# Performance work log

Measured on AMD Instinct MI355X. Metric: run time of the kernel, lower is better.

## Reference

```python
import jax, jax.numpy as jnp
import numpy as np

B, K, N, T, C = 2, 2, 4096, 8, 3
H = 192            # hidden_dim
NODE_DIM = 10
N_LAYERS = 10
KNN = 16           # k nearest neighbours
TOP_FRAC = 0.4
SHARP = 5.0        # mask_sharpness
S = max(int(TOP_FRAC * N), KNN + 1)   # n_select per graph


def _ln(x, g, b, eps=1e-5):
    mu = x.mean(-1, keepdims=True)
    v = ((x - mu) ** 2).mean(-1, keepdims=True)  # biased var, matches nn.LayerNorm
    return (x - mu) / jnp.sqrt(v + eps) * g + b


def setup_inputs() -> dict:
    key = jax.random.key(0)
    ks = jax.random.split(key, 12)
    rn = lambda k, shape: 0.05 * jax.random.normal(k, shape, jnp.float32)
    F0 = 2 * NODE_DIM + 4   # first EdgeConv MLP in-dim
    FR = 2 * H + 4          # remaining EdgeConv MLP in-dim
    L = N_LAYERS - 1
    return {
        "u_base": jax.random.normal(ks[0], (B, K, N, C), jnp.float32),
        "pos": jax.random.uniform(ks[1], (B, N, 3), dtype=jnp.float32),
        "velocity_in": jax.random.normal(ks[2], (B, T, N, C), jnp.float32),
        "airfoil_mask": (jax.random.uniform(ks[3], (B, N)) < 0.05).astype(jnp.float32),
        "conv0_w1": rn(ks[4], (F0, H)), "conv0_b1": jnp.zeros((H,)),
        "conv0_w2": rn(ks[5], (H, H)), "conv0_b2": jnp.zeros((H,)),
        "conv0_g": jnp.ones((H,)), "conv0_be": jnp.zeros((H,)),
        "convs_w1": rn(ks[6], (L, FR, H)), "convs_b1": jnp.zeros((L, H)),
        "convs_w2": rn(ks[7], (L, H, H)), "convs_b2": jnp.zeros((L, H)),
        "convs_g": jnp.ones((L, H)), "convs_be": jnp.zeros((L, H)),
        "head_g": jnp.ones((H,)), "head_be": jnp.zeros((H,)),
        "head_w1": rn(ks[8], (H, H)), "head_b1": jnp.zeros((H,)),
        "head_w2": rn(ks[9], (H, 3)), "head_b2": jnp.zeros((3,)),
    }


def reference(u_base, pos, velocity_in, airfoil_mask,
              conv0_w1, conv0_b1, conv0_w2, conv0_b2, conv0_g, conv0_be,
              convs_w1, convs_b1, convs_w2, convs_b2, convs_g, convs_be,
              head_g, head_be, head_w1, head_b1, head_w2, head_b2):
    # --- variance gating (torch .var/.std are unbiased) ---
    var_pp = jnp.var(velocity_in, axis=1, ddof=1).sum(-1)                      # [B,N]
    var_z = (var_pp - var_pp.mean(1, keepdims=True)) / (
        jnp.std(var_pp, axis=1, ddof=1, keepdims=True) + 1e-8)
    soft_mask = jax.nn.sigmoid(SHARP * var_z) * (1.0 - airfoil_mask)           # [B,N]

    # --- select top-variance points per graph ---
    _, top_idx = jax.lax.top_k(var_pp, S)                                      # [B,S]
    pos_sel = jnp.take_along_axis(pos, top_idx[..., None], axis=1)             # [B,S,3]
    mask_sel = jnp.take_along_axis(soft_mask, top_idx, axis=1)[..., None]      # [B,S,1]
    v_last = velocity_in[:, -1]                                                # [B,N,C]
    ub_sel = jnp.take_along_axis(u_base, top_idx[:, None, :, None], axis=2)    # [B,K,S,C]
    vl_sel = jnp.take_along_axis(v_last, top_idx[..., None], axis=1)           # [B,S,C]
    vf_sel = jnp.take_along_axis(var_pp[..., None], top_idx[..., None], axis=1)
    static = jnp.concatenate([vl_sel, pos_sel, vf_sel], -1)                    # [B,S,7]
    x0 = jnp.concatenate(
        [ub_sel, jnp.broadcast_to(static[:, None], (B, K, S, 7))], -1)         # [B,K,S,10]

    def per_graph(x, pos_b):  # x: [K,S,F0], pos_b: [S,3]
        # kNN graph (self excluded via +inf diagonal, as in the chunked cdist)
        d2 = jnp.sum((pos_b[:, None] - pos_b[None]) ** 2, -1)                  # [S,S]
        d2 = d2.at[jnp.arange(S), jnp.arange(S)].set(jnp.inf)
        _, knn = jax.lax.top_k(-d2, KNN)                                       # [S,KNN]
        # PyG convention with edge_index=stack([targets, sources]):
        # i = edge_index[1] = knn neighbours, j = edge_index[0] = centre nodes
        idx_i = knn.reshape(-1)                     # [E] aggregation targets
        idx_j = jnp.repeat(jnp.arange(S), KNN)      # [E]
        rel = pos_b[idx_i] - pos_b[idx_j]           # pos[edge_index[1]] - pos[edge_index[0]]
        dist = jnp.linalg.norm(rel, axis=-1, keepdims=True)
        ea = jnp.concatenate([rel, dist], -1)       # [E,4]
        ea_b = jnp.broadcast_to(ea, (K,) + ea.shape)

        def conv(h, w1, b1, w2, b2, g, be):
            hi = h[:, idx_i]
            hj = h[:, idx_j]
            m = jnp.concatenate([hi, hj - hi, ea_b], -1)                       # [K,E,2F+4]
            m = jax.nn.gelu(m @ w1 + b1, approximate=False) @ w2 + b2          # [K,E,H]
            agg = jnp.zeros((K, S, H), h.dtype).at[:, idx_i].add(m)
            return _ln(agg, g, be)

        h = conv(x, conv0_w1, conv0_b1, conv0_w2, conv0_b2, conv0_g, conv0_be)
        for l in range(N_LAYERS - 1):
            h = conv(h, convs_w1[l], convs_b1[l], convs_w2[l], convs_b2[l],
                     convs_g[l], convs_be[l]) + h
        hh = _ln(h, head_g, head_be)
        return jax.nn.gelu(hh @ head_w1 + head_b1, approximate=False) @ head_w2 + head_b2

    delta = jax.vmap(per_graph)(x0, pos_sel)        # [B,K,S,3]
    delta = delta * mask_sel[:, None]               # [B,1,S,1]

    def scatter_b(idx, d):  # idx [S], d [K,S,3]
        return jnp.zeros((K, N, C), d.dtype).at[:, idx].set(d)

    delta_full = jax.vmap(scatter_b)(top_idx, delta)            # [B,K,N,C]
    return (u_base + delta_full) * (1.0 - airfoil_mask)[:, None, :, None]
```

## Files before the change

kernel.cpp:

```cpp
#include <hip/hip_runtime.h>
#include <hip/hip_bf16.h>
#include <math.h>

#define B_ 2
#define K_ 2
#define NN_ 4096
#define T_ 8
#define C_ 3
#define H_ 192
#define S_ 1638
#define KK_ 16
#define E_ (S_*KK_)
#define NROW (B_*K_*S_)
#define SHARP_ 5.0f

typedef __hip_bfloat16 bf;
typedef unsigned long long ull;
typedef __bf16 bf16x8 __attribute__((ext_vector_type(8)));
typedef float f32x4 __attribute__((ext_vector_type(4)));

__device__ int   g_isbf16;
__device__ int   g_viol;
__device__ __align__(16) float g_var[B_*NN_];
__device__ __align__(16) float g_accum[B_*2];
__device__ __align__(16) int   g_topidx[B_*S_];
__device__ __align__(16) float g_possel[B_*S_*3];
__device__ __align__(16) float g_masksel[B_*S_];
__device__ __align__(16) float g_x0[NROW*10];
__device__ __align__(16) int   g_knn[B_*E_];
__device__ __align__(16) float g_ea[B_*E_*4];
__device__ __align__(16) int   g_indeg[B_*S_];
__device__ __align__(16) int   g_cursor[B_*S_];
__device__ __align__(16) int   g_off[B_*(S_+1)];
__device__ __align__(16) int   g_list[B_*E_];
__device__ __align__(16) float g_P[(size_t)NROW*H_];
__device__ __align__(16) bf    g_Qbf[(size_t)NROW*H_];
__device__ __align__(16) float g_h[(size_t)NROW*H_];
__device__ __align__(16) bf    g_hbf[(size_t)NROW*H_];
__device__ __align__(16) bf    g_abf[(size_t)NROW*H_];
__device__ __align__(16) bf    g_hh[(size_t)NROW*H_];
__device__ __align__(16) bf    g_t[(size_t)NROW*H_];
__device__ __align__(16) bf    g_w2p[(size_t)11*H_*H_];
__device__ __align__(16) bf    g_wcp[(size_t)9*H_*384];

__device__ __forceinline__ float bf2f(bf x){ return __bfloat162float(x); }
__device__ __forceinline__ float LD(const void* p, long i){
  return g_isbf16 ? __bfloat162float(((const bf*)p)[i]) : ((const float*)p)[i];
}
__device__ __forceinline__ float gelu_f(float x){ return 0.5f*x*(1.0f + erff(x*0.70710678118654752f)); }
__device__ __forceinline__ ull shfl_xor_u64(ull v, int m){
  unsigned lo = (unsigned)v, hi = (unsigned)(v >> 32);
  lo = __shfl_xor(lo, m, 64); hi = __shfl_xor(hi, m, 64);
  return ((ull)hi << 32) | lo;
}

__global__ void k_vz(const void* a, const void* b, const void* c){
  int tid = blockIdx.x*256 + threadIdx.x;
  if (tid < B_*S_){ g_indeg[tid]=0; g_cursor[tid]=0; }
  if (tid < B_*2) g_accum[tid]=0.f;
  if (blockIdx.x == 0){
    int t = threadIdx.x;
    const bf* pa = (const bf*)a; const bf* pb = (const bf*)b; const bf* pc = (const bf*)c;
    int bad = 0;
    #pragma unroll
    for (int s = 0; s < 2; ++s){
      float va = __bfloat162float(pa[t + s*256]);
      float vb = __bfloat162float(pb[t + s*256]);
      float vc = __bfloat162float(pc[t + s*256]);
      if (!(fabsf(va) <= 1000.f)) bad = 1;
      if (!(fabsf(vb) <= 1000.f)) bad = 1;
      if (!(fabsf(vc) <= 1000.f)) bad = 1;
    }
    if (threadIdx.x == 0) g_viol = 0;
    __syncthreads();
    if (bad) atomicOr(&g_viol, 1);
    __syncthreads();
    if (threadIdx.x == 0) g_isbf16 = (g_viol == 0) ? 1 : 0;
  }
}

__global__ void k_var(const void* __restrict__ vel){
  int b = blockIdx.y;
  int n = blockIdx.x*256 + threadIdx.x;
  float v = 0.f;
  #pragma unroll
  for (int c = 0; c < 3; ++c){
    float x[8];
    #pragma unroll
    for (int t = 0; t < 8; ++t)
      x[t] = LD(vel, ((long)(b*T_+t)*NN_ + n)*3 + c);
    float m = __fadd_rn(__fadd_rn(__fadd_rn(x[0],x[1]), __fadd_rn(x[2],x[3])),
                        __fadd_rn(__fadd_rn(x[4],x[5]), __fadd_rn(x[6],x[7]))) / 8.0f;
    float d[8];
    #pragma unroll
    for (int t = 0; t < 8; ++t){ float dd = __fadd_rn(x[t], -m); d[t] = __fmul_rn(dd,dd); }
    float sv = __fadd_rn(__fadd_rn(__fadd_rn(d[0],d[1]), __fadd_rn(d[2],d[3])),
                         __fadd_rn(__fadd_rn(d[4],d[5]), __fadd_rn(d[6],d[7])));
    v = __fadd_rn(v, sv / 7.0f);
  }
  g_var[b*NN_ + n] = v;
  float s1 = v, s2 = v*v;
  #pragma unroll
  for (int o = 32; o; o >>= 1){ s1 += __shfl_xor(s1,o,64); s2 += __shfl_xor(s2,o,64); }
  __shared__ float r1[4], r2[4];
  int lane = threadIdx.x & 63, wid = threadIdx.x >> 6;
  if (!lane){ r1[wid]=s1; r2[wid]=s2; }
  __syncthreads();
  if (threadIdx.x == 0){
    atomicAdd(&g_accum[b*2+0], r1[0]+r1[1]+r1[2]+r1[3]);
    atomicAdd(&g_accum[b*2+1], r2[0]+r2[1]+r2[2]+r2[3]);
  }
}

__global__ __launch_bounds__(256) void k_rank(){
  int b = blockIdx.y;
  int i = blockIdx.x*4 + (threadIdx.x >> 6);
  int lane = threadIdx.x & 63;
  float vi = g_var[b*NN_+i];
  int rank = 0;
  for (int j = lane; j < NN_; j += 64){
    float vj = g_var[b*NN_+j];
    rank += ((vj > vi) || (vj == vi && j < i)) ? 1 : 0;
  }
  #pragma unroll
  for (int o = 32; o; o >>= 1) rank += __shfl_xor(rank, o, 64);
  if (lane == 0 && rank < S_) g_topidx[b*S_ + rank] = i;
}

__global__ void k_gather(const void* __restrict__ pos, const void* __restrict__ ub,
                         const void* __restrict__ vel, const void* __restrict__ air){
  int gi = blockIdx.x*256 + threadIdx.x;
  if (gi >= B_*S_) return;
  int b = gi / S_, s = gi - b*S_;
  int node = g_topidx[gi];
  float px = LD(pos, ((long)b*NN_+node)*3+0);
  float py = LD(pos, ((long)b*NN_+node)*3+1);
  float pz = LD(pos, ((long)b*NN_+node)*3+2);
  g_possel[gi*3+0]=px; g_possel[gi*3+1]=py; g_possel[gi*3+2]=pz;
  float S1 = g_accum[b*2], S2 = g_accum[b*2+1];
  float mean = S1*(1.f/NN_);
  float sd = sqrtf(fmaxf((S2 - S1*S1*(1.f/NN_))*(1.f/(NN_-1)), 0.f));
  float vf = g_var[b*NN_+node];
  float z = (vf-mean)/(sd+1e-8f);
  float sig = 1.f/(1.f+expf(-SHARP_*z));
  g_masksel[gi] = sig*(1.f - LD(air, b*NN_+node));
  float vl0 = LD(vel, ((long)(b*T_+7)*NN_+node)*3+0);
  float vl1 = LD(vel, ((long)(b*T_+7)*NN_+node)*3+1);
  float vl2 = LD(vel, ((long)(b*T_+7)*NN_+node)*3+2);
  for (int k = 0; k < K_; ++k){
    long row = (long)(b*K_+k)*S_ + s;
    float* x = g_x0 + row*10;
    x[0]=LD(ub, ((long)(b*K_+k)*NN_+node)*3+0);
    x[1]=LD(ub, ((long)(b*K_+k)*NN_+node)*3+1);
    x[2]=LD(ub, ((long)(b*K_+k)*NN_+node)*3+2);
    x[3]=vl0; x[4]=vl1; x[5]=vl2;
    x[6]=px;  x[7]=py;  x[8]=pz;
    x[9]=vf;
  }
}

__global__ __launch_bounds__(256) void k_knn(){
  __shared__ float px[S_], py[S_], pz[S_];
  int b = blockIdx.y;
  int j = blockIdx.x*4 + (threadIdx.x >> 6);
  int lane = threadIdx.x & 63;
  for (int t = threadIdx.x; t < S_; t += 256){
    px[t] = g_possel[(b*S_+t)*3+0];
    py[t] = g_possel[(b*S_+t)*3+1];
    pz[t] = g_possel[(b*S_+t)*3+2];
  }
  __syncthreads();
  if (j >= S_) return;
  float xj=px[j], yj=py[j], zj=pz[j];
  float dist[KK_]; int id[KK_];
  #pragma unroll
  for (int t = 0; t < KK_; ++t){ dist[t]=3.0e38f; id[t]=0x7fffffff; }
  for (int c = lane; c < S_; c += 64){
    if (c == j) continue;
    float dx=__fadd_rn(px[c],-xj), dy=__fadd_rn(py[c],-yj), dz=__fadd_rn(pz[c],-zj);
    float d2 = __fadd_rn(__fadd_rn(__fmul_rn(dx,dx), __fmul_rn(dy,dy)), __fmul_rn(dz,dz));
    if (d2 < dist[KK_-1]){
      int p = 0;
      #pragma unroll
      for (int q = 0; q < KK_; ++q) p += (dist[q] <= d2) ? 1 : 0;
      #pragma unroll
      for (int q = KK_-1; q >= 1; --q){
        bool mv = (q > p);
        dist[q] = mv ? dist[q-1] : dist[q];
        id[q]   = mv ? id[q-1]   : id[q];
      }
      #pragma unroll
      for (int q = 0; q < KK_; ++q){ if (q == p){ dist[q] = d2; id[q] = c; } }
    }
  }
  ull mykey = 0;
  #pragma unroll
  for (int t = 0; t < KK_; ++t){
    ull k = (((ull)__float_as_uint(dist[0])) << 32) | (unsigned)id[0];
    ull m = k;
    #pragma unroll
    for (int o = 32; o; o >>= 1){ ull other = shfl_xor_u64(m, o); m = (other < m) ? other : m; }
    if (k == m){
      #pragma unroll
      for (int q = 0; q < KK_-1; ++q){ dist[q]=dist[q+1]; id[q]=id[q+1]; }
      dist[KK_-1] = 3.0e38f; id[KK_-1] = 0x7fffffff;
    }
    if (lane == t) mykey = m;
  }
  if (lane < KK_){
    int i = (int)(mykey & 0xffffffffu);
    g_knn[(b*S_+j)*KK_ + lane] = i;
    float rx = __fadd_rn(px[i],-xj), ry = __fadd_rn(py[i],-yj), rz = __fadd_rn(pz[i],-zj);
    float dd = sqrtf(__fadd_rn(__fadd_rn(__fmul_rn(rx,rx), __fmul_rn(ry,ry)), __fmul_rn(rz,rz)));
    float* o = g_ea + ((long)b*E_ + j*KK_ + lane)*4;
    o[0]=rx; o[1]=ry; o[2]=rz; o[3]=dd;
    atomicAdd(&g_indeg[b*S_+i], 1);
  }
}

__global__ void k_scan(){
  __shared__ int sA[2048], sB[2048];
  int b = blockIdx.x, tid = threadIdx.x;
  for (int i = tid; i < 2048; i += 1024) sA[i] = (i < S_) ? g_indeg[b*S_+i] : 0;
  __syncthreads();
  int *src = sA, *dst = sB;
  for (int d = 1; d < 2048; d <<= 1){
    for (int i = tid; i < 2048; i += 1024) dst[i] = src[i] + (i >= d ? src[i-d] : 0);
    __syncthreads();
    int* t2 = src; src = dst; dst = t2;
  }
  if (tid == 0) g_off[b*(S_+1)] = 0;
  for (int i = tid; i < S_; i += 1024) g_off[b*(S_+1)+i+1] = src[i];
}

__global__ void k_fill(){
  int idx = blockIdx.x*256 + threadIdx.x;
  if (idx >= B_*E_) return;
  int b = idx / E_, e = idx - b*E_;
  int i = g_knn[idx];
  int slot = atomicAdd(&g_cursor[b*S_+i], 1);
  g_list[b*E_ + g_off[b*(S_+1)+i] + slot] = e;
}

__global__ void k_pack_w2(const void* __restrict__ c0w2, const void* __restrict__ cw2,
                          const void* __restrict__ hw1){
  int gi = blockIdx.x*256 + threadIdx.x;
  if (gi >= 11*H_*H_) return;
  int mat = gi / (H_*H_), r = gi - mat*(H_*H_);
  int k = r / H_, n = r - (r/H_)*H_;
  float v;
  if (mat == 0)      v = LD(c0w2, (long)k*H_ + n);
  else if (mat <= 9) v = LD(cw2, (long)(mat-1)*H_*H_ + (long)k*H_ + n);
  else               v = LD(hw1, (long)k*H_ + n);
  int t = k>>5, q = (k>>3)&3, jj = k&7;
  g_w2p[(size_t)mat*H_*H_ + (((t*4+q)*H_ + n)*8 + jj)] = __float2bfloat16(v);
}

__global__ void k_pack_wc(const void* __restrict__ cw1){
  int gi = blockIdx.x*256 + threadIdx.x;
  if (gi >= 9*H_*384) return;
  int l = gi / (H_*384), r = gi - l*(H_*384);
  int k = r / 384, n = r - (r/384)*384;
  long base = (long)l*388*H_;
  float v;
  if (n < H_) v = LD(cw1, base + (long)k*H_ + n) - LD(cw1, base + (long)(H_+k)*H_ + n);
  else        v = LD(cw1, base + (long)(H_+k)*H_ + (n-H_));
  int t = k>>5, q = (k>>3)&3, jj = k&7;
  g_wcp[(size_t)l*(H_*384) + (((t*4+q)*384 + n)*8 + jj)] = __float2bfloat16(v);
}

__global__ void k_initout(const void* __restrict__ ub, const void* __restrict__ air, float* __restrict__ out){
  int gi = blockIdx.x*256 + threadIdx.x;
  int n = (gi/3) % NN_;
  int b = gi / (K_*NN_*C_);
  float a = 1.f - LD(air, b*NN_+n);
  out[gi] = LD(ub, gi) * a;
}

__global__ __launch_bounds__(256) void k_proj0(const void* __restrict__ w1){
  __shared__ float xs[16][10];
  __shared__ float wP[10][192];
  __shared__ float wQ[10][192];
  int tid = threadIdx.x;
  long rowBase = (long)blockIdx.x * 16;
  for (int idx = tid; idx < 1920; idx += 256){
    int f = idx / 192, n = idx - (idx/192)*192;
    float a = LD(w1, f*H_+n), b = LD(w1, (10+f)*H_+n);
    wP[f][n] = a - b; wQ[f][n] = b;
  }
  for (int idx = tid; idx < 160; idx += 256){
    int r = idx / 10, f = idx - (idx/10)*10;
    long row = rowBase + r; if (row >= NROW) row = NROW-1;
    xs[r][f] = g_x0[row*10 + f];
  }
  __syncthreads();
  for (int o = tid; o < 16*384; o += 256){
    int r = o / 384, n = o - (o/384)*384;
    long row = rowBase + r;
    if (row >= NROW) continue;
    float acc = 0.f;
    if (n < 192){
      #pragma unroll
      for (int f = 0; f < 10; ++f) acc += xs[r][f]*wP[f][n];
      g_P[row*192 + n] = acc;
    } else {
      int nc = n - 192;
      #pragma unroll
      for (int f = 0; f < 10; ++f) acc += xs[r][f]*wQ[f][nc];
      g_Qbf[row*192 + nc] = __float2bfloat16(acc);
    }
  }
}

__global__ __launch_bounds__(256) void k_gemmPQ(int bOff, int M){
  const bf* A  = g_hbf;
  const bf* Bp = g_wcp + bOff;
  int wave = threadIdx.x >> 6, lane = threadIdx.x & 63;
  int q = lane >> 4, l16 = lane & 15;
  long rowBase = (long)blockIdx.x * 16;
  f32x4 acc[6];
  #pragma unroll
  for (int ct = 0; ct < 6; ++ct) acc[ct] = (f32x4){0.f,0.f,0.f,0.f};
  #pragma unroll
  for (int t = 0; t < 6; ++t){
    int kof = t*32 + q*8;
    long r = rowBase + l16; if (r >= M) r = M-1;
    bf16x8 af = *reinterpret_cast<const bf16x8*>(A + r*192 + kof);
    #pragma unroll
    for (int ct = 0; ct < 6; ++ct){
      int n = wave*96 + ct*16 + l16;
      bf16x8 bfr = *reinterpret_cast<const bf16x8*>(Bp + (((t*4+q)*384 + n)*8));
      acc[ct] = __builtin_amdgcn_mfma_f32_16x16x32_bf16(af, bfr, acc[ct], 0,0,0);
    }
  }
  #pragma unroll
  for (int ct = 0; ct < 6; ++ct){
    int col = wave*96 + ct*16 + l16;
    #pragma unroll
    for (int r = 0; r < 4; ++r){
      long row = rowBase + q*4 + r;
      if (row < M){
        float v = acc[ct][r];
        if (col < 192) g_P[row*192 + col] = v;
        else           g_Qbf[row*192 + (col-192)] = __float2bfloat16(v);
      }
    }
  }
}

template<int RES>
__global__ __launch_bounds__(256) void k_gemmln(const void* __restrict__ biasB, long biasO,
                                                const void* __restrict__ gB, long gO,
                                                const void* __restrict__ beB, long beO,
                                                int bOff, int M){
  const bf* A  = g_abf;
  const bf* Bp = g_w2p + bOff;
  int wave = threadIdx.x >> 6, lane = threadIdx.x & 63;
  int q = lane >> 4, l16 = lane & 15;
  long rowBase = (long)blockIdx.x * 16;
  f32x4 acc[3];
  #pragma unroll
  for (int ct = 0; ct < 3; ++ct) acc[ct] = (f32x4){0.f,0.f,0.f,0.f};
  #pragma unroll
  for (int t = 0; t < 6; ++t){
    int kof = t*32 + q*8;
    long r = rowBase + l16; if (r >= M) r = M-1;
    bf16x8 af = *reinterpret_cast<const bf16x8*>(A + r*192 + kof);
    #pragma unroll
    for (int ct = 0; ct < 3; ++ct){
      int n = wave*48 + ct*16 + l16;
      bf16x8 bfr = *reinterpret_cast<const bf16x8*>(Bp + (((t*4+q)*192 + n)*8));
      acc[ct] = __builtin_amdgcn_mfma_f32_16x16x32_bf16(af, bfr, acc[ct], 0,0,0);
    }
  }
  __shared__ float tile[16][200];
  __shared__ float srow[16], rrow[16];
  #pragma unroll
  for (int ct = 0; ct < 3; ++ct){
    int col = wave*48 + ct*16 + l16;
    float bb = LD(biasB, biasO + col);
    #pragma unroll
    for (int r = 0; r < 4; ++r){
      int lr = q*4 + r;
      long row = rowBase + lr;
      long rowc = (row < M) ? row : (M-1);
      int bk = (int)(rowc / S_); int i = (int)(rowc - (long)bk*S_); int b = bk >> 1;
      float degf = (float)(g_off[b*(S_+1)+i+1] - g_off[b*(S_+1)+i]);
      tile[lr][col] = acc[ct][r] + degf*bb;
    }
  }
  __syncthreads();
  {
    int lr = threadIdx.x >> 4;
    int k16 = threadIdx.x & 15;
    float s = 0.f, qq = 0.f;
    for (int c = k16; c < 192; c += 16){ float x = tile[lr][c]; s += x; qq += x*x; }
    #pragma unroll
    for (int o = 1; o < 16; o <<= 1){ s += __shfl_xor(s,o,64); qq += __shfl_xor(qq,o,64); }
    if (k16 == 0){
      float mu = s*(1.f/H_);
      float var = qq*(1.f/H_) - mu*mu;
      srow[lr] = mu;
      rrow[lr] = rsqrtf(fmaxf(var, 0.f) + 1e-5f);
    }
  }
  __syncthreads();
  for (int o = threadIdx.x; o < 16*192; o += 256){
    int lr = o / 192, col = o - (o/192)*192;
    long row = rowBase + lr;
    if (row < M){
      float y = (tile[lr][col] - srow[lr])*rrow[lr]*LD(gB,gO+col) + LD(beB,beO+col);
      if (RES) y += g_h[row*192 + col];
      g_h[row*192 + col] = y;
      g_hbf[row*192 + col] = __float2bfloat16(y);
    }
  }
}

__global__ __launch_bounds__(256) void k_gemmhead(const void* __restrict__ gB,
                                                  const void* __restrict__ beB,
                                                  const void* __restrict__ biasB,
                                                  int bOff, int M){
  const bf* Bp = g_w2p + bOff;
  int wave = threadIdx.x >> 6, lane = threadIdx.x & 63;
  int q = lane >> 4, l16 = lane & 15;
  long rowBase = (long)blockIdx.x * 32;
  __shared__ float tile[32][200];
  __shared__ bf hb_s[32][216];
  __shared__ float srow[32], rrow[32];
  for (int o = threadIdx.x; o < 32*192; o += 256){
    int lr = o / 192, col = o - (o/192)*192;
    long row = rowBase + lr;
    long rowc = (row < M) ? row : (M-1);
    tile[lr][col] = g_h[rowc*192 + col];
  }
  __syncthreads();
  {
    int lr = threadIdx.x >> 3;
    int k8 = threadIdx.x & 7;
    float s = 0.f, qq = 0.f;
    for (int c = k8; c < 192; c += 8){ float x = tile[lr][c]; s += x; qq += x*x; }
    #pragma unroll
    for (int o = 1; o < 8; o <<= 1){ s += __shfl_xor(s,o,64); qq += __shfl_xor(qq,o,64); }
    if (k8 == 0){
      float mu = s*(1.f/H_);
      float var = qq*(1.f/H_) - mu*mu;
      srow[lr] = mu;
      rrow[lr] = rsqrtf(fmaxf(var, 0.f) + 1e-5f);
    }
  }
  __syncthreads();
  for (int o = threadIdx.x; o < 32*192; o += 256){
    int lr = o / 192, col = o - (o/192)*192;
    hb_s[lr][col] = __float2bfloat16((tile[lr][col] - srow[lr])*rrow[lr]*LD(gB,col) + LD(beB,col));
  }
  __syncthreads();
  f32x4 acc[2][3];
  #pragma unroll
  for (int rt = 0; rt < 2; ++rt)
    #pragma unroll
    for (int ct = 0; ct < 3; ++ct) acc[rt][ct] = (f32x4){0.f,0.f,0.f,0.f};
  #pragma unroll
  for (int t = 0; t < 6; ++t){
    int kof = t*32 + q*8;
    bf16x8 af[2], bfr[3];
    #pragma unroll
    for (int rt = 0; rt < 2; ++rt)
      af[rt] = *reinterpret_cast<const bf16x8*>(&hb_s[rt*16 + l16][kof]);
    #pragma unroll
    for (int ct = 0; ct < 3; ++ct){
      int n = wave*48 + ct*16 + l16;
      bfr[ct] = *reinterpret_cast<const bf16x8*>(Bp + (((t*4+q)*192 + n)*8));
    }
    #pragma unroll
    for (int rt = 0; rt < 2; ++rt)
      #pragma unroll
      for (int ct = 0; ct < 3; ++ct)
        acc[rt][ct] = __builtin_amdgcn_mfma_f32_16x16x32_bf16(af[rt], bfr[ct], acc[rt][ct], 0,0,0);
  }
  #pragma unroll
  for (int rt = 0; rt < 2; ++rt){
    #pragma unroll
    for (int ct = 0; ct < 3; ++ct){
      int col = wave*48 + ct*16 + l16;
      float bb = LD(biasB, col);
      #pragma unroll
      for (int r = 0; r < 4; ++r){
        long row = rowBase + rt*16 + q*4 + r;
        if (row < M) g_t[row*192 + col] = __float2bfloat16(gelu_f(acc[rt][ct][r] + bb));
      }
    }
  }
}

__global__ __launch_bounds__(192) void k_aggedge(const void* __restrict__ w1cB, long w1cO,
                                                 const void* __restrict__ b1B, long b1O){
  int row = blockIdx.x;
  int col = threadIdx.x;
  int bk = row / S_, i = row - bk*S_, b = bk >> 1;
  int off = g_off[b*(S_+1)+i];
  int deg = g_off[b*(S_+1)+i+1] - off;
  float w0 = LD(w1cB, w1cO+col),       w1v = LD(w1cB, w1cO+H_+col);
  float w2v = LD(w1cB, w1cO+2*H_+col), w3v = LD(w1cB, w1cO+3*H_+col);
  float base = g_P[(size_t)row*H_ + col] + LD(b1B, b1O+col);
  const int* lst = g_list + b*E_ + off;
  const bf* Q = g_Qbf + (size_t)bk*S_*H_;
  const float* EA = g_ea + (size_t)b*E_*4;
  float acc = 0.f;
  int d = 0;
  for (; d + 4 <= deg; d += 4){
    int e0 = lst[d], e1 = lst[d+1], e2 = lst[d+2], e3 = lst[d+3];
    float4 a0 = *reinterpret_cast<const float4*>(EA + (size_t)e0*4);
    float4 a1 = *reinterpret_cast<const float4*>(EA + (size_t)e1*4);
    float4 a2 = *reinterpret_cast<const float4*>(EA + (size_t)e2*4);
    float4 a3 = *reinterpret_cast<const float4*>(EA + (size_t)e3*4);
    float q0 = bf2f(Q[(size_t)(e0>>4)*H_ + col]);
    float q1 = bf2f(Q[(size_t)(e1>>4)*H_ + col]);
    float q2 = bf2f(Q[(size_t)(e2>>4)*H_ + col]);
    float q3 = bf2f(Q[(size_t)(e3>>4)*H_ + col]);
    acc += gelu_f(base + q0 + a0.x*w0 + a0.y*w1v + a0.z*w2v + a0.w*w3v);
    acc += gelu_f(base + q1 + a1.x*w0 + a1.y*w1v + a1.z*w2v + a1.w*w3v);
    acc += gelu_f(base + q2 + a2.x*w0 + a2.y*w1v + a2.z*w2v + a2.w*w3v);
    acc += gelu_f(base + q3 + a3.x*w0 + a3.y*w1v + a3.z*w2v + a3.w*w3v);
  }
  for (; d < deg; ++d){
    int e = lst[d];
    float4 a = *reinterpret_cast<const float4*>(EA + (size_t)e*4);
    float qv = bf2f(Q[(size_t)(e>>4)*H_ + col]);
    acc += gelu_f(base + qv + a.x*w0 + a.y*w1v + a.z*w2v + a.w*w3v);
  }
  g_abf[(size_t)row*H_ + col] = __float2bfloat16(acc);
}

__global__ void k_headout(const void* __restrict__ w2, const void* __restrict__ b2,
                          const void* __restrict__ ub, const void* __restrict__ air,
                          float* __restrict__ out){
  int row = blockIdx.x*4 + (threadIdx.x >> 6);
  int lane = threadIdx.x & 63;
  if (row >= NROW) return;
  float t0 = bf2f(g_t[(size_t)row*H_ + lane]);
  float t1 = bf2f(g_t[(size_t)row*H_ + lane + 64]);
  float t2 = bf2f(g_t[(size_t)row*H_ + lane + 128]);
  float d[3];
  #pragma unroll
  for (int c = 0; c < 3; ++c){
    float p = t0*LD(w2,lane*3+c) + t1*LD(w2,(lane+64)*3+c) + t2*LD(w2,(lane+128)*3+c);
    #pragma unroll
    for (int o = 32; o; o >>= 1) p += __shfl_xor(p,o,64);
    d[c] = p + LD(b2,c);
  }
  if (lane == 0){
    int bk = row / S_, s = row - bk*S_, b = bk >> 1;
    float msk = g_masksel[b*S_+s];
    int node = g_topidx[b*S_+s];
    float am = 1.f - LD(air, b*NN_+node);
    #pragma unroll
    for (int c = 0; c < 3; ++c){
      long oi = ((long)bk*NN_ + node)*3 + c;
      out[oi] = (LD(ub,oi) + d[c]*msk)*am;
    }
  }
}

extern "C" void kernel_launch(void* const* d_in, const int* in_sizes, int n_in,
                              void* d_out, int out_size, void* d_ws, size_t ws_size,
                              hipStream_t stream) {
  (void)in_sizes; (void)n_in; (void)d_ws; (void)ws_size; (void)out_size;
  const void* u_base = d_in[0];
  const void* pos    = d_in[1];
  const void* vel    = d_in[2];
  const void* air    = d_in[3];
  const void* c0w1   = d_in[4];
  const void* c0b1   = d_in[5];
  const void* c0w2   = d_in[6];
  const void* c0b2   = d_in[7];
  const void* c0g    = d_in[8];
  const void* c0be   = d_in[9];
  const void* cw1    = d_in[10];
  const void* cb1    = d_in[11];
  const void* cw2    = d_in[12];
  const void* cb2    = d_in[13];
  const void* cg     = d_in[14];
  const void* cbe    = d_in[15];
  const void* hg     = d_in[16];
  const void* hbe    = d_in[17];
  const void* hw1    = d_in[18];
  const void* hb1    = d_in[19];
  const void* hw2    = d_in[20];
  const void* hb2    = d_in[21];
  float* out = (float*)d_out;

  k_vz<<<13, 256, 0, stream>>>(u_base, pos, vel);
  k_var<<<dim3(16, B_), 256, 0, stream>>>(vel);
  k_rank<<<dim3(NN_/4, B_), 256, 0, stream>>>();
  k_gather<<<13, 256, 0, stream>>>(pos, u_base, vel, air);
  k_knn<<<dim3((S_+3)/4, B_), 256, 0, stream>>>();
  k_scan<<<B_, 1024, 0, stream>>>();
  k_fill<<<205, 256, 0, stream>>>();
  k_pack_w2<<<1584, 256, 0, stream>>>(c0w2, cw2, hw1);
  k_pack_wc<<<2592, 256, 0, stream>>>(cw1);
  k_initout<<<192, 256, 0, stream>>>(u_base, air, out);
  k_proj0<<<410, 256, 0, stream>>>(c0w1);

  const int GN16 = (NROW + 15) / 16;
  for (int l = 0; l < 10; ++l){
    if (l > 0) k_gemmPQ<<<GN16, 256, 0, stream>>>((l-1)*H_*384, NROW);

    long w1cO = (l == 0) ? 20L*H_ : ((long)(l-1)*388 + 384)*H_;
    const void* w1cB = (l == 0) ? c0w1 : cw1;
    long lOff = (l == 0) ? 0 : (long)(l-1)*H_;
    const void* b1B = (l == 0) ? c0b1 : cb1;
    k_aggedge<<<NROW, 192, 0, stream>>>(w1cB, w1cO, b1B, lOff);

    const void* b2B = (l == 0) ? c0b2 : cb2;
    const void* gB  = (l == 0) ? c0g  : cg;
    const void* beB = (l == 0) ? c0be : cbe;
    if (l > 0) k_gemmln<1><<<GN16, 256, 0, stream>>>(b2B, lOff, gB, lOff, beB, lOff, l*H_*H_, NROW);
    else       k_gemmln<0><<<GN16, 256, 0, stream>>>(b2B, lOff, gB, lOff, beB, lOff, l*H_*H_, NROW);
  }

  k_gemmhead<<<(NROW + 31)/32, 256, 0, stream>>>(hg, hbe, hb1, 10*H_*H_, NROW);
  k_headout<<<NROW/4, 256, 0, stream>>>(hw2, hb2, u_base, air, out);
}
```

Baseline: 659.6 us.

## Fuse next-layer PQ GEMM into LayerNorm kernel and fold head output into head GEMM

The next layer's P/Q projection GEMM now runs inside the LayerNorm kernel, reading the freshly normalized rows from shared memory as bf16 instead of writing g_hbf and launching a separate k_gemmPQ. The final 192->3 head projection and output scatter are fused into the head GEMM kernel, which drops the g_t buffer and the k_headout launch. The dtype check and zeroing move into k_var, which writes per-block partial sums instead of using atomics. The weight pack and output init kernels are merged into one launch. Together this cuts launch count and global round trips, at the cost of more shared memory and registers in the fused kernels.

```diff
diff --git a/kernel.cpp b/kernel.cpp
--- a/kernel.cpp
+++ b/kernel.cpp
@@ -20,9 +20,9 @@
 typedef float f32x4 __attribute__((ext_vector_type(4)));
 
 __device__ int   g_isbf16;
-__device__ int   g_viol;
 __device__ __align__(16) float g_var[B_*NN_];
-__device__ __align__(16) float g_accum[B_*2];
+__device__ __align__(16) float g_vs1[B_*16];
+__device__ __align__(16) float g_vs2[B_*16];
 __device__ __align__(16) int   g_topidx[B_*S_];
 __device__ __align__(16) float g_possel[B_*S_*3];
 __device__ __align__(16) float g_masksel[B_*S_];
@@ -36,16 +36,16 @@
 __device__ __align__(16) float g_P[(size_t)NROW*H_];
 __device__ __align__(16) bf    g_Qbf[(size_t)NROW*H_];
 __device__ __align__(16) float g_h[(size_t)NROW*H_];
-__device__ __align__(16) bf    g_hbf[(size_t)NROW*H_];
 __device__ __align__(16) bf    g_abf[(size_t)NROW*H_];
-__device__ __align__(16) bf    g_hh[(size_t)NROW*H_];
-__device__ __align__(16) bf    g_t[(size_t)NROW*H_];
 __device__ __align__(16) bf    g_w2p[(size_t)11*H_*H_];
 __device__ __align__(16) bf    g_wcp[(size_t)9*H_*384];
 
 __device__ __forceinline__ float bf2f(bf x){ return __bfloat162float(x); }
 __device__ __forceinline__ float LD(const void* p, long i){
   return g_isbf16 ? __bfloat162float(((const bf*)p)[i]) : ((const float*)p)[i];
+}
+__device__ __forceinline__ float LDi(const void* p, long i, int isb){
+  return isb ? __bfloat162float(((const bf*)p)[i]) : ((const float*)p)[i];
 }
 __device__ __forceinline__ float gelu_f(float x){ return 0.5f*x*(1.0f + erff(x*0.70710678118654752f)); }
 __device__ __forceinline__ ull shfl_xor_u64(ull v, int m){
@@ -54,41 +54,42 @@
   return ((ull)hi << 32) | lo;
 }
 
-__global__ void k_vz(const void* a, const void* b, const void* c){
-  int tid = blockIdx.x*256 + threadIdx.x;
-  if (tid < B_*S_){ g_indeg[tid]=0; g_cursor[tid]=0; }
-  if (tid < B_*2) g_accum[tid]=0.f;
-  if (blockIdx.x == 0){
-    int t = threadIdx.x;
-    const bf* pa = (const bf*)a; const bf* pb = (const bf*)b; const bf* pc = (const bf*)c;
+__global__ __launch_bounds__(256) void k_var(const void* __restrict__ vel,
+                                             const void* __restrict__ ub,
+                                             const void* __restrict__ pos){
+  __shared__ int s_bad;
+  int b = blockIdx.y;
+  int bx = blockIdx.x;
+  int tid = threadIdx.x;
+  if (tid == 0) s_bad = 0;
+  __syncthreads();
+  {
+    const bf* pa = (const bf*)ub; const bf* pb = (const bf*)pos; const bf* pc = (const bf*)vel;
     int bad = 0;
     #pragma unroll
     for (int s = 0; s < 2; ++s){
-      float va = __bfloat162float(pa[t + s*256]);
-      float vb = __bfloat162float(pb[t + s*256]);
-      float vc = __bfloat162float(pc[t + s*256]);
+      float va = __bfloat162float(pa[tid + s*256]);
+      float vb = __bfloat162float(pb[tid + s*256]);
+      float vc = __bfloat162float(pc[tid + s*256]);
       if (!(fabsf(va) <= 1000.f)) bad = 1;
       if (!(fabsf(vb) <= 1000.f)) bad = 1;
       if (!(fabsf(vc) <= 1000.f)) bad = 1;
     }
-    if (threadIdx.x == 0) g_viol = 0;
-    __syncthreads();
-    if (bad) atomicOr(&g_viol, 1);
-    __syncthreads();
-    if (threadIdx.x == 0) g_isbf16 = (g_viol == 0) ? 1 : 0;
-  }
-}
-
-__global__ void k_var(const void* __restrict__ vel){
-  int b = blockIdx.y;
-  int n = blockIdx.x*256 + threadIdx.x;
+    if (bad) atomicOr(&s_bad, 1);
+  }
+  __syncthreads();
+  int isb = (s_bad == 0) ? 1 : 0;
+  if (bx == 0 && b == 0 && tid == 0) g_isbf16 = isb;
+  int zi = (b*16 + bx)*256 + tid;
+  if (zi < B_*S_){ g_indeg[zi] = 0; g_cursor[zi] = 0; }
+  int n = bx*256 + tid;
   float v = 0.f;
   #pragma unroll
   for (int c = 0; c < 3; ++c){
     float x[8];
     #pragma unroll
     for (int t = 0; t < 8; ++t)
-      x[t] = LD(vel, ((long)(b*T_+t)*NN_ + n)*3 + c);
+      x[t] = LDi(vel, ((long)(b*T_+t)*NN_ + n)*3 + c, isb);
     float m = __fadd_rn(__fadd_rn(__fadd_rn(x[0],x[1]), __fadd_rn(x[2],x[3])),
                         __fadd_rn(__fadd_rn(x[4],x[5]), __fadd_rn(x[6],x[7]))) / 8.0f;
     float d[8];
@@ -103,12 +104,12 @@
   #pragma unroll
   for (int o = 32; o; o >>= 1){ s1 += __shfl_xor(s1,o,64); s2 += __shfl_xor(s2,o,64); }
   __shared__ float r1[4], r2[4];
-  int lane = threadIdx.x & 63, wid = threadIdx.x >> 6;
+  int lane = tid & 63, wid = tid >> 6;
   if (!lane){ r1[wid]=s1; r2[wid]=s2; }
   __syncthreads();
-  if (threadIdx.x == 0){
-    atomicAdd(&g_accum[b*2+0], r1[0]+r1[1]+r1[2]+r1[3]);
-    atomicAdd(&g_accum[b*2+1], r2[0]+r2[1]+r2[2]+r2[3]);
+  if (tid == 0){
+    g_vs1[b*16 + bx] = r1[0]+r1[1]+r1[2]+r1[3];
+    g_vs2[b*16 + bx] = r2[0]+r2[1]+r2[2]+r2[3];
   }
 }
 
@@ -137,7 +138,9 @@
   float py = LD(pos, ((long)b*NN_+node)*3+1);
   float pz = LD(pos, ((long)b*NN_+node)*3+2);
   g_possel[gi*3+0]=px; g_possel[gi*3+1]=py; g_possel[gi*3+2]=pz;
-  float S1 = g_accum[b*2], S2 = g_accum[b*2+1];
+  float S1 = 0.f, S2 = 0.f;
+  #pragma unroll
+  for (int t = 0; t < 16; ++t){ S1 += g_vs1[b*16+t]; S2 += g_vs2[b*16+t]; }
   float mean = S1*(1.f/NN_);
   float sd = sqrtf(fmaxf((S2 - S1*S1*(1.f/NN_))*(1.f/(NN_-1)), 0.f));
   float vf = g_var[b*NN_+node];
@@ -242,39 +245,43 @@
   g_list[b*E_ + g_off[b*(S_+1)+i] + slot] = e;
 }
 
-__global__ void k_pack_w2(const void* __restrict__ c0w2, const void* __restrict__ cw2,
-                          const void* __restrict__ hw1){
-  int gi = blockIdx.x*256 + threadIdx.x;
-  if (gi >= 11*H_*H_) return;
-  int mat = gi / (H_*H_), r = gi - mat*(H_*H_);
-  int k = r / H_, n = r - (r/H_)*H_;
-  float v;
-  if (mat == 0)      v = LD(c0w2, (long)k*H_ + n);
-  else if (mat <= 9) v = LD(cw2, (long)(mat-1)*H_*H_ + (long)k*H_ + n);
-  else               v = LD(hw1, (long)k*H_ + n);
-  int t = k>>5, q = (k>>3)&3, jj = k&7;
-  g_w2p[(size_t)mat*H_*H_ + (((t*4+q)*H_ + n)*8 + jj)] = __float2bfloat16(v);
-}
-
-__global__ void k_pack_wc(const void* __restrict__ cw1){
-  int gi = blockIdx.x*256 + threadIdx.x;
-  if (gi >= 9*H_*384) return;
-  int l = gi / (H_*384), r = gi - l*(H_*384);
-  int k = r / 384, n = r - (r/384)*384;
-  long base = (long)l*388*H_;
-  float v;
-  if (n < H_) v = LD(cw1, base + (long)k*H_ + n) - LD(cw1, base + (long)(H_+k)*H_ + n);
-  else        v = LD(cw1, base + (long)(H_+k)*H_ + (n-H_));
-  int t = k>>5, q = (k>>3)&3, jj = k&7;
-  g_wcp[(size_t)l*(H_*384) + (((t*4+q)*384 + n)*8 + jj)] = __float2bfloat16(v);
-}
-
-__global__ void k_initout(const void* __restrict__ ub, const void* __restrict__ air, float* __restrict__ out){
-  int gi = blockIdx.x*256 + threadIdx.x;
-  int n = (gi/3) % NN_;
-  int b = gi / (K_*NN_*C_);
-  float a = 1.f - LD(air, b*NN_+n);
-  out[gi] = LD(ub, gi) * a;
+#define PW2_BLKS 1584
+#define PWC_BLKS 2592
+#define INIT_BLKS 192
+__global__ void k_packall(const void* __restrict__ c0w2, const void* __restrict__ cw2,
+                          const void* __restrict__ hw1, const void* __restrict__ cw1,
+                          const void* __restrict__ ub, const void* __restrict__ air,
+                          float* __restrict__ out){
+  int blk = blockIdx.x;
+  if (blk < PW2_BLKS){
+    int gi = blk*256 + threadIdx.x;
+    if (gi >= 11*H_*H_) return;
+    int mat = gi / (H_*H_), r = gi - mat*(H_*H_);
+    int k = r / H_, n = r - (r/H_)*H_;
+    float v;
+    if (mat == 0)      v = LD(c0w2, (long)k*H_ + n);
+    else if (mat <= 9) v = LD(cw2, (long)(mat-1)*H_*H_ + (long)k*H_ + n);
+    else               v = LD(hw1, (long)k*H_ + n);
+    int t = k>>5, q = (k>>3)&3, jj = k&7;
+    g_w2p[(size_t)mat*H_*H_ + (((t*4+q)*H_ + n)*8 + jj)] = __float2bfloat16(v);
+  } else if (blk < PW2_BLKS + PWC_BLKS){
+    int gi = (blk - PW2_BLKS)*256 + threadIdx.x;
+    if (gi >= 9*H_*384) return;
+    int l = gi / (H_*384), r = gi - l*(H_*384);
+    int k = r / 384, n = r - (r/384)*384;
+    long base = (long)l*388*H_;
+    float v;
+    if (n < H_) v = LD(cw1, base + (long)k*H_ + n) - LD(cw1, base + (long)(H_+k)*H_ + n);
+    else        v = LD(cw1, base + (long)(H_+k)*H_ + (n-H_));
+    int t = k>>5, q = (k>>3)&3, jj = k&7;
+    g_wcp[(size_t)l*(H_*384) + (((t*4+q)*384 + n)*8 + jj)] = __float2bfloat16(v);
+  } else {
+    int gi = (blk - PW2_BLKS - PWC_BLKS)*256 + threadIdx.x;
+    int n = (gi/3) % NN_;
+    int b = gi / (K_*NN_*C_);
+    float a = 1.f - LD(air, b*NN_+n);
+    out[gi] = LD(ub, gi) * a;
+  }
 }
 
 __global__ __launch_bounds__(256) void k_proj0(const void* __restrict__ w1){
@@ -312,47 +319,11 @@
   }
 }
 
-__global__ __launch_bounds__(256) void k_gemmPQ(int bOff, int M){
-  const bf* A  = g_hbf;
-  const bf* Bp = g_wcp + bOff;
-  int wave = threadIdx.x >> 6, lane = threadIdx.x & 63;
-  int q = lane >> 4, l16 = lane & 15;
-  long rowBase = (long)blockIdx.x * 16;
-  f32x4 acc[6];
-  #pragma unroll
-  for (int ct = 0; ct < 6; ++ct) acc[ct] = (f32x4){0.f,0.f,0.f,0.f};
-  #pragma unroll
-  for (int t = 0; t < 6; ++t){
-    int kof = t*32 + q*8;
-    long r = rowBase + l16; if (r >= M) r = M-1;
-    bf16x8 af = *reinterpret_cast<const bf16x8*>(A + r*192 + kof);
-    #pragma unroll
-    for (int ct = 0; ct < 6; ++ct){
-      int n = wave*96 + ct*16 + l16;
-      bf16x8 bfr = *reinterpret_cast<const bf16x8*>(Bp + (((t*4+q)*384 + n)*8));
-      acc[ct] = __builtin_amdgcn_mfma_f32_16x16x32_bf16(af, bfr, acc[ct], 0,0,0);
-    }
-  }
-  #pragma unroll
-  for (int ct = 0; ct < 6; ++ct){
-    int col = wave*96 + ct*16 + l16;
-    #pragma unroll
-    for (int r = 0; r < 4; ++r){
-      long row = rowBase + q*4 + r;
-      if (row < M){
-        float v = acc[ct][r];
-        if (col < 192) g_P[row*192 + col] = v;
-        else           g_Qbf[row*192 + (col-192)] = __float2bfloat16(v);
-      }
-    }
-  }
-}
-
-template<int RES>
-__global__ __launch_bounds__(256) void k_gemmln(const void* __restrict__ biasB, long biasO,
-                                                const void* __restrict__ gB, long gO,
-                                                const void* __restrict__ beB, long beO,
-                                                int bOff, int M){
+template<int RES, int DOPQ>
+__global__ __launch_bounds__(256) void k_lnpq(const void* __restrict__ biasB, long biasO,
+                                              const void* __restrict__ gB, long gO,
+                                              const void* __restrict__ beB, long beO,
+                                              int bOff, int pqOff, int M){
   const bf* A  = g_abf;
   const bf* Bp = g_w2p + bOff;
   int wave = threadIdx.x >> 6, lane = threadIdx.x & 63;
@@ -374,6 +345,7 @@
     }
   }
   __shared__ float tile[16][200];
+  __shared__ bf    ybf[16][200];
   __shared__ float srow[16], rrow[16];
   #pragma unroll
   for (int ct = 0; ct < 3; ++ct){
@@ -408,19 +380,54 @@
   for (int o = threadIdx.x; o < 16*192; o += 256){
     int lr = o / 192, col = o - (o/192)*192;
     long row = rowBase + lr;
-    if (row < M){
-      float y = (tile[lr][col] - srow[lr])*rrow[lr]*LD(gB,gO+col) + LD(beB,beO+col);
-      if (RES) y += g_h[row*192 + col];
-      g_h[row*192 + col] = y;
-      g_hbf[row*192 + col] = __float2bfloat16(y);
-    }
-  }
-}
-
-__global__ __launch_bounds__(256) void k_gemmhead(const void* __restrict__ gB,
-                                                  const void* __restrict__ beB,
-                                                  const void* __restrict__ biasB,
-                                                  int bOff, int M){
+    long rowc = (row < M) ? row : (M-1);
+    float y = (tile[lr][col] - srow[lr])*rrow[lr]*LD(gB,gO+col) + LD(beB,beO+col);
+    if (RES) y += g_h[rowc*192 + col];
+    if (row < M) g_h[row*192 + col] = y;
+    ybf[lr][col] = __float2bfloat16(y);
+  }
+  if (DOPQ){
+    __syncthreads();
+    const bf* Bq = g_wcp + pqOff;
+    f32x4 acc2[6];
+    #pragma unroll
+    for (int ct = 0; ct < 6; ++ct) acc2[ct] = (f32x4){0.f,0.f,0.f,0.f};
+    #pragma unroll
+    for (int t = 0; t < 6; ++t){
+      int kof = t*32 + q*8;
+      bf16x8 af = *reinterpret_cast<const bf16x8*>(&ybf[l16][kof]);
+      #pragma unroll
+      for (int ct = 0; ct < 6; ++ct){
+        int n = wave*96 + ct*16 + l16;
+        bf16x8 bfr = *reinterpret_cast<const bf16x8*>(Bq + (((t*4+q)*384 + n)*8));
+        acc2[ct] = __builtin_amdgcn_mfma_f32_16x16x32_bf16(af, bfr, acc2[ct], 0,0,0);
+      }
+    }
+    #pragma unroll
+    for (int ct = 0; ct < 6; ++ct){
+      int col = wave*96 + ct*16 + l16;
+      #pragma unroll
+      for (int r = 0; r < 4; ++r){
+        long row = rowBase + q*4 + r;
+        if (row < M){
+          float v = acc2[ct][r];
+          if (col < 192) g_P[row*192 + col] = v;
+          else           g_Qbf[row*192 + (col-192)] = __float2bfloat16(v);
+        }
+      }
+    }
+  }
+}
+
+__global__ __launch_bounds__(256) void k_head(const void* __restrict__ gB,
+                                              const void* __restrict__ beB,
+                                              const void* __restrict__ biasB,
+                                              const void* __restrict__ w2,
+                                              const void* __restrict__ b2,
+                                              const void* __restrict__ ubase,
+                                              const void* __restrict__ air,
+                                              float* __restrict__ out,
+                                              int bOff, int M){
   const bf* Bp = g_w2p + bOff;
   int wave = threadIdx.x >> 6, lane = threadIdx.x & 63;
   int q = lane >> 4, l16 = lane & 15;
@@ -486,9 +493,38 @@
       float bb = LD(biasB, col);
       #pragma unroll
       for (int r = 0; r < 4; ++r){
-        long row = rowBase + rt*16 + q*4 + r;
-        if (row < M) g_t[row*192 + col] = __float2bfloat16(gelu_f(acc[rt][ct][r] + bb));
+        int lr = rt*16 + q*4 + r;
+        tile[lr][col] = gelu_f(acc[rt][ct][r] + bb);
       }
+    }
+  }
+  __syncthreads();
+  {
+    int r = threadIdx.x >> 3, k8 = threadIdx.x & 7;
+    long row = rowBase + r;
+    float p0 = 0.f, p1 = 0.f, p2 = 0.f;
+    for (int col = k8; col < 192; col += 8){
+      float tv = tile[r][col];
+      p0 += tv*LD(w2, col*3+0);
+      p1 += tv*LD(w2, col*3+1);
+      p2 += tv*LD(w2, col*3+2);
+    }
+    #pragma unroll
+    for (int o = 1; o < 8; o <<= 1){
+      p0 += __shfl_xor(p0,o,64);
+      p1 += __shfl_xor(p1,o,64);
+      p2 += __shfl_xor(p2,o,64);
+    }
+    if (k8 == 0 && row < M){
+      int bk = (int)(row / S_), s = (int)(row - (long)bk*S_), b = bk >> 1;
+      float msk = g_masksel[b*S_+s];
+      int node = g_topidx[b*S_+s];
+      float am = 1.f - LD(air, b*NN_+node);
+      float d0 = p0 + LD(b2,0), d1 = p1 + LD(b2,1), d2 = p2 + LD(b2,2);
+      long oi = ((long)bk*NN_ + node)*3;
+      out[oi+0] = (LD(ubase, oi+0) + d0*msk)*am;
+      out[oi+1] = (LD(ubase, oi+1) + d1*msk)*am;
+      out[oi+2] = (LD(ubase, oi+2) + d2*msk)*am;
     }
   }
 }
@@ -532,36 +568,6 @@
   g_abf[(size_t)row*H_ + col] = __float2bfloat16(acc);
 }
 
-__global__ void k_headout(const void* __restrict__ w2, const void* __restrict__ b2,
-                          const void* __restrict__ ub, const void* __restrict__ air,
-                          float* __restrict__ out){
-  int row = blockIdx.x*4 + (threadIdx.x >> 6);
-  int lane = threadIdx.x & 63;
-  if (row >= NROW) return;
-  float t0 = bf2f(g_t[(size_t)row*H_ + lane]);
-  float t1 = bf2f(g_t[(size_t)row*H_ + lane + 64]);
-  float t2 = bf2f(g_t[(size_t)row*H_ + lane + 128]);
-  float d[3];
-  #pragma unroll
-  for (int c = 0; c < 3; ++c){
-    float p = t0*LD(w2,lane*3+c) + t1*LD(w2,(lane+64)*3+c) + t2*LD(w2,(lane+128)*3+c);
-    #pragma unroll
-    for (int o = 32; o; o >>= 1) p += __shfl_xor(p,o,64);
-    d[c] = p + LD(b2,c);
-  }
-  if (lane == 0){
-    int bk = row / S_, s = row - bk*S_, b = bk >> 1;
-    float msk = g_masksel[b*S_+s];
-    int node = g_topidx[b*S_+s];
-    float am = 1.f - LD(air, b*NN_+node);
-    #pragma unroll
-    for (int c = 0; c < 3; ++c){
-      long oi = ((long)bk*NN_ + node)*3 + c;
-      out[oi] = (LD(ub,oi) + d[c]*msk)*am;
-    }
-  }
-}
-
 extern "C" void kernel_launch(void* const* d_in, const int* in_sizes, int n_in,
                               void* d_out, int out_size, void* d_ws, size_t ws_size,
                               hipStream_t stream) {
@@ -590,22 +596,17 @@
   const void* hb2    = d_in[21];
   float* out = (float*)d_out;
 
-  k_vz<<<13, 256, 0, stream>>>(u_base, pos, vel);
-  k_var<<<dim3(16, B_), 256, 0, stream>>>(vel);
+  k_var<<<dim3(16, B_), 256, 0, stream>>>(vel, u_base, pos);
   k_rank<<<dim3(NN_/4, B_), 256, 0, stream>>>();
   k_gather<<<13, 256, 0, stream>>>(pos, u_base, vel, air);
   k_knn<<<dim3((S_+3)/4, B_), 256, 0, stream>>>();
   k_scan<<<B_, 1024, 0, stream>>>();
   k_fill<<<205, 256, 0, stream>>>();
-  k_pack_w2<<<1584, 256, 0, stream>>>(c0w2, cw2, hw1);
-  k_pack_wc<<<2592, 256, 0, stream>>>(cw1);
-  k_initout<<<192, 256, 0, stream>>>(u_base, air, out);
+  k_packall<<<PW2_BLKS + PWC_BLKS + INIT_BLKS, 256, 0, stream>>>(c0w2, cw2, hw1, cw1, u_base, air, out);
   k_proj0<<<410, 256, 0, stream>>>(c0w1);
 
   const int GN16 = (NROW + 15) / 16;
   for (int l = 0; l < 10; ++l){
-    if (l > 0) k_gemmPQ<<<GN16, 256, 0, stream>>>((l-1)*H_*384, NROW);
-
     long w1cO = (l == 0) ? 20L*H_ : ((long)(l-1)*388 + 384)*H_;
     const void* w1cB = (l == 0) ? c0w1 : cw1;
     long lOff = (l == 0) ? 0 : (long)(l-1)*H_;
@@ -615,10 +616,13 @@
     const void* b2B = (l == 0) ? c0b2 : cb2;
     const void* gB  = (l == 0) ? c0g  : cg;
     const void* beB = (l == 0) ? c0be : cbe;
-    if (l > 0) k_gemmln<1><<<GN16, 256, 0, stream>>>(b2B, lOff, gB, lOff, beB, lOff, l*H_*H_, NROW);
-    else       k_gemmln<0><<<GN16, 256, 0, stream>>>(b2B, lOff, gB, lOff, beB, lOff, l*H_*H_, NROW);
-  }
-
-  k_gemmhead<<<(NROW + 31)/32, 256, 0, stream>>>(hg, hbe, hb1, 10*H_*H_, NROW);
-  k_headout<<<NROW/4, 256, 0, stream>>>(hw2, hb2, u_base, air, out);
-}
+    if (l == 0)
+      k_lnpq<0,1><<<GN16, 256, 0, stream>>>(b2B, lOff, gB, lOff, beB, lOff, 0,        0,         NROW);
+    else if (l < 9)
+      k_lnpq<1,1><<<GN16, 256, 0, stream>>>(b2B, lOff, gB, lOff, beB, lOff, l*H_*H_, l*H_*384,  NROW);
+    else
+      k_lnpq<1,0><<<GN16, 256, 0, stream>>>(b2B, lOff, gB, lOff, beB, lOff, l*H_*H_, 0,         NROW);
+  }
+
+  k_head<<<(NROW + 31)/32, 256, 0, stream>>>(hg, hbe, hb1, hw2, hb2, u_base, air, out, 10*H_*H_, NROW);
+}
```

Measured after the change: 617.8 us. -6.3%, faster.
